# Optimization experiments

Hardware: AMD Instinct MI355X
Metric: run time of the kernel (lower is better)

Reference implementation:

```python
import jax, jax.numpy as jnp
import numpy as np

N, E, D = 50000, 1600000, 32
P = 2.0  # exponent self.p


def setup_inputs() -> dict:
    key = jax.random.key(0)
    k1, k2, k3 = jax.random.split(key, 3)
    X = jax.random.normal(k1, (N, D), dtype=jnp.float32)
    edge_index = jax.random.randint(k2, (2, E), 0, N)
    W = jax.random.normal(k3, (D, D), dtype=jnp.float32) / np.float32(np.sqrt(D))
    b = jnp.zeros((D,), dtype=jnp.float32)
    return {"X": X, "edge_index": edge_index, "W": W, "b": b}


def gcn_conv(X, edge_index, W, b, n):
    # PyG GCNConv: add self-loops, symmetric deg^-1/2 normalization,
    # aggregate messages from source col -> target row.
    src, dst = edge_index[0], edge_index[1]
    loops = jnp.arange(n)
    row = jnp.concatenate([dst, loops])  # targets
    col = jnp.concatenate([src, loops])  # sources
    deg = jax.ops.segment_sum(jnp.ones(row.shape, X.dtype), row, num_segments=n)
    dinv = jax.lax.rsqrt(jnp.maximum(deg, 1.0))  # deg >= 1 (self-loops)
    h = X @ W  # [N, D]
    msg = h[col] * (dinv[col] * dinv[row])[:, None]  # [E+N, D]
    return jax.ops.segment_sum(msg, row, num_segments=n) + b


def reference(X, edge_index, W, b):
    n = X.shape[0]
    h = jax.nn.relu(gcn_conv(X, edge_index, W, b, n))  # activation(conv(X, ei))
    src, dst = edge_index[0], edge_index[1]
    e = jnp.abs(h[src] - h[dst]) ** P  # [E, D] gather + pow
    s = jax.ops.segment_sum(e, src, num_segments=n)  # scatter-sum by source
    cnt = jax.ops.segment_sum(jnp.ones((e.shape[0],), h.dtype), src, num_segments=n)
    mean = s / jnp.maximum(cnt, 1.0)[:, None]  # scatter-mean finalize
    return jnp.tanh(mean)
```

## Files before the change

kernel.cpp:

```cpp
#include <hip/hip_runtime.h>

#define D 32
#define CSH 7
#define KMASK 127
#define PSH 23
#define PMASK ((1u << PSH) - 1u)
#define NBMAX 512

typedef unsigned int uint;

__device__ inline uint bf16rne(float f) {
    uint u = __float_as_uint(f);
    return (u + 0x7FFFu + ((u >> 16) & 1u)) >> 16;
}
__device__ inline float bf_lo(uint w) { return __uint_as_float(w << 16); }
__device__ inline float bf_hi(uint w) { return __uint_as_float(w & 0xFFFF0000u); }
__device__ inline uint bf_pack(float x, float y) { return bf16rne(x) | (bf16rne(y) << 16); }

__global__ void zero_kernel(int* __restrict__ p, int n) {
    int i = threadIdx.x;
    if (i < n) p[i] = 0;
}

__global__ void coarse_scatter(const int* __restrict__ src, const int* __restrict__ dst,
                               int* __restrict__ gCurD, int* __restrict__ gCurS,
                               uint* __restrict__ coarseD, uint* __restrict__ coarseS,
                               int E, int cap) {
    __shared__ int hD[NBMAX], hS[NBMAX], baseD[NBMAX], baseS[NBMAX];
    int t = threadIdx.x;
    if (t < NBMAX) { hD[t] = 0; hS[t] = 0; }
    __syncthreads();
    int s[4], d[4], lpD[4], lpS[4];
    int j0 = blockIdx.x * 4096 + 4 * t;
    int nv = 0;
    if (j0 + 3 < E) {
        int4 s4 = *(const int4*)(src + j0);
        int4 d4 = *(const int4*)(dst + j0);
        s[0] = s4.x; s[1] = s4.y; s[2] = s4.z; s[3] = s4.w;
        d[0] = d4.x; d[1] = d4.y; d[2] = d4.z; d[3] = d4.w;
        nv = 4;
    } else {
        for (int u = 0; u < 4; ++u) {
            int j = j0 + u;
            if (j < E) { s[nv] = src[j]; d[nv] = dst[j]; ++nv; }
        }
    }
    for (int u = 0; u < nv; ++u) {
        lpD[u] = atomicAdd(&hD[d[u] >> CSH], 1);
        lpS[u] = atomicAdd(&hS[s[u] >> CSH], 1);
    }
    __syncthreads();
    if (t < NBMAX) {
        if (hD[t]) baseD[t] = atomicAdd(&gCurD[t], hD[t]);
        if (hS[t]) baseS[t] = atomicAdd(&gCurS[t], hS[t]);
    }
    __syncthreads();
    for (int u = 0; u < nv; ++u) {
        int bD = d[u] >> CSH, relD = baseD[bD] + lpD[u];
        if (relD < cap)
            coarseD[(size_t)bD * cap + relD] = ((uint)(d[u] & KMASK) << PSH) | (uint)s[u];
        int bS = s[u] >> CSH, relS = baseS[bS] + lpS[u];
        if (relS < cap)
            coarseS[(size_t)bS * cap + relS] = ((uint)(s[u] & KMASK) << PSH) | (uint)d[u];
    }
}

__global__ void fineD_build(const uint* __restrict__ coarseD, const int* __restrict__ gCurD,
                            int* __restrict__ rowStartD, int* __restrict__ rowEndD,
                            int* __restrict__ adjD, float* __restrict__ dinv,
                            int N, int cap) {
    __shared__ int cnt[128];
    __shared__ int pre[128];
    int b = blockIdx.x;
    int t = threadIdx.x;
    int nodeLo = b << CSH;
    int nNodes = min(128, N - nodeLo);
    if (t < 128) cnt[t] = 0;
    __syncthreads();
    size_t lo = (size_t)b * cap;
    int n = min(gCurD[b], cap - 512);
    int n4 = n >> 2;
    const uint4* c4 = (const uint4*)(coarseD + lo);
    for (int kk = t; kk < n4; kk += 1024) {
        uint4 e4 = c4[kk];
        atomicAdd(&cnt[e4.x >> PSH], 1);
        atomicAdd(&cnt[e4.y >> PSH], 1);
        atomicAdd(&cnt[e4.z >> PSH], 1);
        atomicAdd(&cnt[e4.w >> PSH], 1);
    }
    for (int kk = 4 * n4 + t; kk < n; kk += 1024)
        atomicAdd(&cnt[coarseD[lo + kk] >> PSH], 1);
    __syncthreads();
    int mydeg = 0, mypad = 0;
    if (t < 128) { mydeg = cnt[t]; mypad = (mydeg + 3) & ~3; pre[t] = mypad; }
    __syncthreads();
    for (int off = 1; off < 128; off <<= 1) {
        int x = 0;
        if (t < 128 && t >= off) x = pre[t - off];
        __syncthreads();
        if (t < 128) pre[t] += x;
        __syncthreads();
    }
    int myexcl = 0;
    if (t < 128) myexcl = pre[t] - mypad;
    if (t < nNodes) {
        rowStartD[nodeLo + t] = (int)lo + myexcl;
        rowEndD[nodeLo + t]   = (int)lo + myexcl + mydeg;
        dinv[nodeLo + t] = rsqrtf((float)(mydeg + 1));
    }
    __syncthreads();
    if (t < 128) cnt[t] = (int)lo + myexcl;
    __syncthreads();
    int hiGuard = (int)lo + cap;
    for (int kk = t; kk < n; kk += 1024) {
        uint e = coarseD[lo + kk];
        int pos = atomicAdd(&cnt[e >> PSH], 1);
        if (pos < hiGuard) adjD[pos] = (int)(e & PMASK);
    }
}

__global__ void matmul_scale_kernel(const float* __restrict__ X, const float* __restrict__ W,
                                    const float* __restrict__ dinv, uint* __restrict__ hs16,
                                    int N) {
    __shared__ float Wl[D * D];
    __shared__ float Xl[8 * D];
    int tid = threadIdx.x;
    for (int k = tid; k < D * D; k += 256) Wl[k] = W[k];
    int row0 = blockIdx.x * 8;
    int g = row0 * D + tid;
    Xl[tid] = (g < N * D) ? X[g] : 0.f;
    __syncthreads();
    int r = tid >> 5;
    int d = tid & 31;
    int row = row0 + r;
    float acc = 0.f;
    #pragma unroll
    for (int k = 0; k < D; ++k) acc += Xl[r * D + k] * Wl[k * D + d];
    if (row < N) acc *= dinv[row];
    float other = __shfl_xor(acc, 1);
    if (row < N && (d & 1) == 0)
        hs16[row * 16 + (d >> 1)] = bf_pack(acc, other);
}

__global__ void conv_gather_kernel(const int* __restrict__ rowStartD, const int* __restrict__ rowEndD,
                                   const int* __restrict__ adjD,
                                   const uint* __restrict__ hs16, const float* __restrict__ dinv,
                                   const float* __restrict__ b, uint* __restrict__ h2_16, int N) {
    int node = blockIdx.x * 8 + (threadIdx.x >> 6);
    if (node >= N) return;
    int lane = threadIdx.x & 63;
    int p = lane & 15;
    int slot = lane >> 4;
    int s = rowStartD[node], e = rowEndD[node];
    float ax0 = 0.f, ay0 = 0.f, ax1 = 0.f, ay1 = 0.f;
    float ax2 = 0.f, ay2 = 0.f, ax3 = 0.f, ay3 = 0.f;
    int k = s;
    for (; k + 15 < e; k += 16) {
        int4 iv = *(const int4*)(adjD + k + slot * 4);
        uint w0 = hs16[iv.x * 16 + p];
        uint w1 = hs16[iv.y * 16 + p];
        uint w2 = hs16[iv.z * 16 + p];
        uint w3 = hs16[iv.w * 16 + p];
        ax0 += bf_lo(w0); ay0 += bf_hi(w0);
        ax1 += bf_lo(w1); ay1 += bf_hi(w1);
        ax2 += bf_lo(w2); ay2 += bf_hi(w2);
        ax3 += bf_lo(w3); ay3 += bf_hi(w3);
    }
    for (; k < e; k += 4) {
        int kk = k + slot;
        if (kk < e) {
            uint w = hs16[adjD[kk] * 16 + p];
            ax0 += bf_lo(w); ay0 += bf_hi(w);
        }
    }
    float accx = (ax0 + ax1) + (ax2 + ax3);
    float accy = (ay0 + ay1) + (ay2 + ay3);
    accx += __shfl_xor(accx, 16); accy += __shfl_xor(accy, 16);
    accx += __shfl_xor(accx, 32); accy += __shfl_xor(accy, 32);
    if (slot == 0) {
        uint wself = hs16[node * 16 + p];
        float di = dinv[node];
        float vx = di * (accx + bf_lo(wself)) + b[2 * p];
        float vy = di * (accy + bf_hi(wself)) + b[2 * p + 1];
        h2_16[node * 16 + p] = bf_pack(fmaxf(vx, 0.f), fmaxf(vy, 0.f));
    }
}

__global__ void __launch_bounds__(1024)
pow_fused(const uint* __restrict__ coarseS, const int* __restrict__ gCurS,
          const uint* __restrict__ h2_16, float* __restrict__ out, int N, int cap) {
    extern __shared__ uint adjL[];
    __shared__ int cnt[128];
    __shared__ int pre[128];
    __shared__ int rs[128];
    __shared__ int degL[128];
    __shared__ uint self[128 * 16];
    int b = blockIdx.x;
    int t = threadIdx.x;
    int nodeLo = b << CSH;
    int nNodes = min(128, N - nodeLo);
    if (t < 128) cnt[t] = 0;
    for (int i = t; i < nNodes * 16; i += 1024)
        self[i] = h2_16[(size_t)(nodeLo + (i >> 4)) * 16 + (i & 15)];
    __syncthreads();
    size_t lo = (size_t)b * cap;
    int n = min(gCurS[b], cap - 512);
    int n4 = n >> 2;
    const uint4* c4 = (const uint4*)(coarseS + lo);
    for (int kk = t; kk < n4; kk += 1024) {
        uint4 e4 = c4[kk];
        atomicAdd(&cnt[e4.x >> PSH], 1);
        atomicAdd(&cnt[e4.y >> PSH], 1);
        atomicAdd(&cnt[e4.z >> PSH], 1);
        atomicAdd(&cnt[e4.w >> PSH], 1);
    }
    for (int kk = 4 * n4 + t; kk < n; kk += 1024)
        atomicAdd(&cnt[coarseS[lo + kk] >> PSH], 1);
    __syncthreads();
    int mydeg = 0, mypad = 0;
    if (t < 128) { mydeg = cnt[t]; mypad = (mydeg + 3) & ~3; pre[t] = mypad; }
    __syncthreads();
    for (int off = 1; off < 128; off <<= 1) {
        int x = 0;
        if (t < 128 && t >= off) x = pre[t - off];
        __syncthreads();
        if (t < 128) pre[t] += x;
        __syncthreads();
    }
    if (t < 128) {
        rs[t] = pre[t] - mypad;
        degL[t] = mydeg;
        cnt[t] = pre[t] - mypad;
    }
    __syncthreads();
    for (int kk = t; kk < n; kk += 1024) {
        uint e = coarseS[lo + kk];
        int pos = atomicAdd(&cnt[e >> PSH], 1);
        if (pos < cap) adjL[pos] = e & PMASK;
    }
    __syncthreads();
    int wave = t >> 6, lane = t & 63;
    int p = lane & 15, slot = lane >> 4;
    for (int nl = wave; nl < nNodes; nl += 16) {
        int s = rs[nl];
        int e = s + degL[nl];
        uint wh = self[nl * 16 + p];
        float hx = bf_lo(wh), hy = bf_hi(wh);
        float ax0 = 0.f, ay0 = 0.f, ax1 = 0.f, ay1 = 0.f;
        float ax2 = 0.f, ay2 = 0.f, ax3 = 0.f, ay3 = 0.f;
        int k = s;
        for (; k + 15 < e; k += 16) {
            uint4 iv = *(const uint4*)(adjL + k + slot * 4);
            uint w0 = h2_16[iv.x * 16 + p];
            uint w1 = h2_16[iv.y * 16 + p];
            uint w2 = h2_16[iv.z * 16 + p];
            uint w3 = h2_16[iv.w * 16 + p];
            float vx0 = hx - bf_lo(w0), vy0 = hy - bf_hi(w0);
            float vx1 = hx - bf_lo(w1), vy1 = hy - bf_hi(w1);
            float vx2 = hx - bf_lo(w2), vy2 = hy - bf_hi(w2);
            float vx3 = hx - bf_lo(w3), vy3 = hy - bf_hi(w3);
            ax0 += vx0 * vx0; ay0 += vy0 * vy0;
            ax1 += vx1 * vx1; ay1 += vy1 * vy1;
            ax2 += vx2 * vx2; ay2 += vy2 * vy2;
            ax3 += vx3 * vx3; ay3 += vy3 * vy3;
        }
        for (; k < e; k += 4) {
            int kk = k + slot;
            if (kk < e) {
                uint w = h2_16[adjL[kk] * 16 + p];
                float vx = hx - bf_lo(w), vy = hy - bf_hi(w);
                ax0 += vx * vx; ay0 += vy * vy;
            }
        }
        float accx = (ax0 + ax1) + (ax2 + ax3);
        float accy = (ay0 + ay1) + (ay2 + ay3);
        accx += __shfl_xor(accx, 16); accy += __shfl_xor(accy, 16);
        accx += __shfl_xor(accx, 32); accy += __shfl_xor(accy, 32);
        if (slot == 0) {
            float c = fmaxf((float)degL[nl], 1.f);
            float2 r;
            r.x = tanhf(accx / c);
            r.y = tanhf(accy / c);
            ((float2*)out)[(size_t)(nodeLo + nl) * 16 + p] = r;
        }
    }
}

__global__ void fb_count(const int* __restrict__ src, const int* __restrict__ dst,
                         int* __restrict__ degI, int* __restrict__ cntI, int E) {
    int j = blockIdx.x * blockDim.x + threadIdx.x;
    if (j < E) {
        atomicAdd(&degI[dst[j]], 1);
        atomicAdd(&cntI[src[j]], 1);
    }
}
__global__ void fb_dinv(const int* __restrict__ degI, float* __restrict__ dinv, int N) {
    int i = blockIdx.x * blockDim.x + threadIdx.x;
    if (i < N) dinv[i] = rsqrtf((float)(degI[i] + 1));
}
__global__ void fb_matmul(const float* __restrict__ X, const float* __restrict__ W,
                          const float* __restrict__ dinv, float* __restrict__ hs, int N) {
    __shared__ float Wl[D * D];
    __shared__ float Xl[8 * D];
    int tid = threadIdx.x;
    for (int k = tid; k < D * D; k += 256) Wl[k] = W[k];
    int row0 = blockIdx.x * 8;
    int g = row0 * D + tid;
    Xl[tid] = (g < N * D) ? X[g] : 0.f;
    __syncthreads();
    int r = tid >> 5;
    int d = tid & 31;
    int row = row0 + r;
    if (row < N) {
        float acc = 0.f;
        #pragma unroll
        for (int k = 0; k < D; ++k) acc += Xl[r * D + k] * Wl[k * D + d];
        hs[row * D + d] = acc * dinv[row];
    }
}
__global__ void fb_scatter_conv(const int* __restrict__ src, const int* __restrict__ dst,
                                const float* __restrict__ hs, float* __restrict__ S, int ED) {
    int idx = blockIdx.x * blockDim.x + threadIdx.x;
    if (idx < ED) {
        int j = idx >> 5, d = idx & 31;
        atomicAdd(&S[dst[j] * D + d], hs[src[j] * D + d]);
    }
}
__global__ void fb_h2(float* __restrict__ S, const float* __restrict__ hs,
                      const float* __restrict__ dinv, const float* __restrict__ b, int ND) {
    int idx = blockIdx.x * blockDim.x + threadIdx.x;
    if (idx < ND) {
        int i = idx >> 5, d = idx & 31;
        float v = dinv[i] * (S[idx] + hs[idx]) + b[d];
        S[idx] = fmaxf(v, 0.f);
    }
}
__global__ void fb_edge_pow(const int* __restrict__ src, const int* __restrict__ dst,
                            const float* __restrict__ h2, float* __restrict__ out, int ED) {
    int idx = blockIdx.x * blockDim.x + threadIdx.x;
    if (idx < ED) {
        int j = idx >> 5, d = idx & 31;
        float v = h2[src[j] * D + d] - h2[dst[j] * D + d];
        atomicAdd(&out[src[j] * D + d], v * v);
    }
}
__global__ void fb_finalize(float* __restrict__ out, const int* __restrict__ cntI, int ND) {
    int idx = blockIdx.x * blockDim.x + threadIdx.x;
    if (idx < ND) {
        int i = idx >> 5;
        float c = fmaxf((float)cntI[i], 1.f);
        out[idx] = tanhf(out[idx] / c);
    }
}

extern "C" void kernel_launch(void* const* d_in, const int* in_sizes, int n_in,
                              void* d_out, int out_size, void* d_ws, size_t ws_size,
                              hipStream_t stream) {
    const float* X  = (const float*)d_in[0];
    const int*   ei = (const int*)d_in[1];
    const float* W  = (const float*)d_in[2];
    const float* b  = (const float*)d_in[3];
    int N = in_sizes[0] / D;
    int E = in_sizes[1] / 2;
    const int* src = ei;
    const int* dst = ei + E;
    float* out = (float*)d_out;

    size_t ND = (size_t)N * D;
    size_t NH = (size_t)N * 16;
    int nb = (N + 127) >> CSH;
    int cap = ((E + nb - 1) / nb + 1024 + 15) & ~15;
    size_t capSz = (size_t)nb * cap;
    size_t ldsBytes = (size_t)cap * 4;

    uint* coarseD = (uint*)d_ws;
    uint* coarseS = coarseD + capSz;
    int* adjD = (int*)(coarseS + capSz);
    uint* hs16   = (uint*)(adjD + capSz);
    uint* h2_16  = hs16 + NH;
    float* dinv = (float*)(h2_16 + NH);
    int* rowStartD = (int*)(dinv + N);
    int* rowEndD   = rowStartD + N;
    int* gCurD  = rowEndD + N;
    int* gCurS  = gCurD + NBMAX;
    size_t need = (3 * capSz + 2 * NH + 3 * (size_t)N + 2 * NBMAX) * 4;

    if (ws_size >= need && nb <= NBMAX && N <= (1 << PSH) && capSz < (1u << 30)
        && ldsBytes <= 96 * 1024) {
        zero_kernel<<<1, 1024, 0, stream>>>(gCurD, 2 * NBMAX);
        int cgrid = (E + 4095) / 4096;
        coarse_scatter<<<cgrid, 1024, 0, stream>>>(src, dst, gCurD, gCurS,
                                                   coarseD, coarseS, E, cap);
        fineD_build<<<nb, 1024, 0, stream>>>(coarseD, gCurD, rowStartD, rowEndD,
                                             adjD, dinv, N, cap);
        matmul_scale_kernel<<<(N + 7) / 8, 256, 0, stream>>>(X, W, dinv, hs16, N);
        conv_gather_kernel<<<(N + 7) / 8, 512, 0, stream>>>(rowStartD, rowEndD, adjD,
                                                            hs16, dinv, b, h2_16, N);
        pow_fused<<<nb, 1024, ldsBytes, stream>>>(coarseS, gCurS, h2_16, out, N, cap);
    } else {
        float* fhs  = (float*)d_ws;
        float* S    = fhs + ND;
        float* fdv  = S + ND;
        int*   fdeg = (int*)(fdv + N);
        int*   fcnt = fdeg + N;
        hipMemsetAsync(S, 0, ND * sizeof(float), stream);
        hipMemsetAsync(fdeg, 0, (size_t)2 * N * sizeof(int), stream);
        hipMemsetAsync(d_out, 0, ND * sizeof(float), stream);
        int EDi = E * D, NDi = (int)ND;
        fb_count<<<(E + 255) / 256, 256, 0, stream>>>(src, dst, fdeg, fcnt, E);
        fb_dinv<<<(N + 255) / 256, 256, 0, stream>>>(fdeg, fdv, N);
        fb_matmul<<<(N + 7) / 8, 256, 0, stream>>>(X, W, fdv, fhs, N);
        fb_scatter_conv<<<(EDi + 255) / 256, 256, 0, stream>>>(src, dst, fhs, S, EDi);
        fb_h2<<<(NDi + 255) / 256, 256, 0, stream>>>(S, fhs, fdv, b, NDi);
        fb_edge_pow<<<(EDi + 255) / 256, 256, 0, stream>>>(src, dst, S, out, EDi);
        fb_finalize<<<(NDi + 255) / 256, 256, 0, stream>>>(out, fcnt, NDi);
    }
}
```

Measured before the change: 109.7 us.

## Fuse CSR fine-bucket build into conv gather using LDS adjacency

```diff
diff --git a/kernel.cpp b/kernel.cpp
--- a/kernel.cpp
+++ b/kernel.cpp
@@ -65,16 +65,10 @@
     }
 }
 
-__global__ void fineD_build(const uint* __restrict__ coarseD, const int* __restrict__ gCurD,
-                            int* __restrict__ rowStartD, int* __restrict__ rowEndD,
-                            int* __restrict__ adjD, float* __restrict__ dinv,
-                            int N, int cap) {
+__global__ void deg_dinv_kernel(const uint* __restrict__ coarseD, const int* __restrict__ gCurD,
+                                float* __restrict__ dinv, int N, int cap) {
     __shared__ int cnt[128];
-    __shared__ int pre[128];
-    int b = blockIdx.x;
-    int t = threadIdx.x;
-    int nodeLo = b << CSH;
-    int nNodes = min(128, N - nodeLo);
+    int b = blockIdx.x, t = threadIdx.x;
     if (t < 128) cnt[t] = 0;
     __syncthreads();
     size_t lo = (size_t)b * cap;
@@ -91,32 +85,8 @@
     for (int kk = 4 * n4 + t; kk < n; kk += 1024)
         atomicAdd(&cnt[coarseD[lo + kk] >> PSH], 1);
     __syncthreads();
-    int mydeg = 0, mypad = 0;
-    if (t < 128) { mydeg = cnt[t]; mypad = (mydeg + 3) & ~3; pre[t] = mypad; }
-    __syncthreads();
-    for (int off = 1; off < 128; off <<= 1) {
-        int x = 0;
-        if (t < 128 && t >= off) x = pre[t - off];
-        __syncthreads();
-        if (t < 128) pre[t] += x;
-        __syncthreads();
-    }
-    int myexcl = 0;
-    if (t < 128) myexcl = pre[t] - mypad;
-    if (t < nNodes) {
-        rowStartD[nodeLo + t] = (int)lo + myexcl;
-        rowEndD[nodeLo + t]   = (int)lo + myexcl + mydeg;
-        dinv[nodeLo + t] = rsqrtf((float)(mydeg + 1));
-    }
-    __syncthreads();
-    if (t < 128) cnt[t] = (int)lo + myexcl;
-    __syncthreads();
-    int hiGuard = (int)lo + cap;
-    for (int kk = t; kk < n; kk += 1024) {
-        uint e = coarseD[lo + kk];
-        int pos = atomicAdd(&cnt[e >> PSH], 1);
-        if (pos < hiGuard) adjD[pos] = (int)(e & PMASK);
-    }
+    int node = (b << CSH) + t;
+    if (t < 128 && node < N) dinv[node] = rsqrtf((float)(cnt[t] + 1));
 }
 
 __global__ void matmul_scale_kernel(const float* __restrict__ X, const float* __restrict__ W,
@@ -142,47 +112,95 @@
         hs16[row * 16 + (d >> 1)] = bf_pack(acc, other);
 }
 
-__global__ void conv_gather_kernel(const int* __restrict__ rowStartD, const int* __restrict__ rowEndD,
-                                   const int* __restrict__ adjD,
-                                   const uint* __restrict__ hs16, const float* __restrict__ dinv,
-                                   const float* __restrict__ b, uint* __restrict__ h2_16, int N) {
-    int node = blockIdx.x * 8 + (threadIdx.x >> 6);
-    if (node >= N) return;
-    int lane = threadIdx.x & 63;
-    int p = lane & 15;
-    int slot = lane >> 4;
-    int s = rowStartD[node], e = rowEndD[node];
-    float ax0 = 0.f, ay0 = 0.f, ax1 = 0.f, ay1 = 0.f;
-    float ax2 = 0.f, ay2 = 0.f, ax3 = 0.f, ay3 = 0.f;
-    int k = s;
-    for (; k + 15 < e; k += 16) {
-        int4 iv = *(const int4*)(adjD + k + slot * 4);
-        uint w0 = hs16[iv.x * 16 + p];
-        uint w1 = hs16[iv.y * 16 + p];
-        uint w2 = hs16[iv.z * 16 + p];
-        uint w3 = hs16[iv.w * 16 + p];
-        ax0 += bf_lo(w0); ay0 += bf_hi(w0);
-        ax1 += bf_lo(w1); ay1 += bf_hi(w1);
-        ax2 += bf_lo(w2); ay2 += bf_hi(w2);
-        ax3 += bf_lo(w3); ay3 += bf_hi(w3);
-    }
-    for (; k < e; k += 4) {
-        int kk = k + slot;
-        if (kk < e) {
-            uint w = hs16[adjD[kk] * 16 + p];
-            ax0 += bf_lo(w); ay0 += bf_hi(w);
-        }
-    }
-    float accx = (ax0 + ax1) + (ax2 + ax3);
-    float accy = (ay0 + ay1) + (ay2 + ay3);
-    accx += __shfl_xor(accx, 16); accy += __shfl_xor(accy, 16);
-    accx += __shfl_xor(accx, 32); accy += __shfl_xor(accy, 32);
-    if (slot == 0) {
-        uint wself = hs16[node * 16 + p];
-        float di = dinv[node];
-        float vx = di * (accx + bf_lo(wself)) + b[2 * p];
-        float vy = di * (accy + bf_hi(wself)) + b[2 * p + 1];
-        h2_16[node * 16 + p] = bf_pack(fmaxf(vx, 0.f), fmaxf(vy, 0.f));
+__global__ void __launch_bounds__(1024)
+conv_fused(const uint* __restrict__ coarseD, const int* __restrict__ gCurD,
+           const uint* __restrict__ hs16, const float* __restrict__ bias,
+           uint* __restrict__ h2_16, int N, int cap) {
+    extern __shared__ uint adjL[];
+    __shared__ int cnt[128];
+    __shared__ int pre[128];
+    __shared__ int rs[128];
+    __shared__ int degL[128];
+    int b = blockIdx.x;
+    int t = threadIdx.x;
+    int nodeLo = b << CSH;
+    int nNodes = min(128, N - nodeLo);
+    if (t < 128) cnt[t] = 0;
+    __syncthreads();
+    size_t lo = (size_t)b * cap;
+    int n = min(gCurD[b], cap - 512);
+    int n4 = n >> 2;
+    const uint4* c4 = (const uint4*)(coarseD + lo);
+    for (int kk = t; kk < n4; kk += 1024) {
+        uint4 e4 = c4[kk];
+        atomicAdd(&cnt[e4.x >> PSH], 1);
+        atomicAdd(&cnt[e4.y >> PSH], 1);
+        atomicAdd(&cnt[e4.z >> PSH], 1);
+        atomicAdd(&cnt[e4.w >> PSH], 1);
+    }
+    for (int kk = 4 * n4 + t; kk < n; kk += 1024)
+        atomicAdd(&cnt[coarseD[lo + kk] >> PSH], 1);
+    __syncthreads();
+    int mydeg = 0, mypad = 0;
+    if (t < 128) { mydeg = cnt[t]; mypad = (mydeg + 3) & ~3; pre[t] = mypad; }
+    __syncthreads();
+    for (int off = 1; off < 128; off <<= 1) {
+        int x = 0;
+        if (t < 128 && t >= off) x = pre[t - off];
+        __syncthreads();
+        if (t < 128) pre[t] += x;
+        __syncthreads();
+    }
+    if (t < 128) {
+        rs[t] = pre[t] - mypad;
+        degL[t] = mydeg;
+        cnt[t] = pre[t] - mypad;
+    }
+    __syncthreads();
+    for (int kk = t; kk < n; kk += 1024) {
+        uint e = coarseD[lo + kk];
+        int pos = atomicAdd(&cnt[e >> PSH], 1);
+        if (pos < cap) adjL[pos] = e & PMASK;
+    }
+    __syncthreads();
+    int wave = t >> 6, lane = t & 63;
+    int p = lane & 15, slot = lane >> 4;
+    for (int nl = wave; nl < nNodes; nl += 16) {
+        int s = rs[nl];
+        int e = s + degL[nl];
+        float ax0 = 0.f, ay0 = 0.f, ax1 = 0.f, ay1 = 0.f;
+        float ax2 = 0.f, ay2 = 0.f, ax3 = 0.f, ay3 = 0.f;
+        int k = s;
+        for (; k + 15 < e; k += 16) {
+            uint4 iv = *(const uint4*)(adjL + k + slot * 4);
+            uint w0 = hs16[iv.x * 16 + p];
+            uint w1 = hs16[iv.y * 16 + p];
+            uint w2 = hs16[iv.z * 16 + p];
+            uint w3 = hs16[iv.w * 16 + p];
+            ax0 += bf_lo(w0); ay0 += bf_hi(w0);
+            ax1 += bf_lo(w1); ay1 += bf_hi(w1);
+            ax2 += bf_lo(w2); ay2 += bf_hi(w2);
+            ax3 += bf_lo(w3); ay3 += bf_hi(w3);
+        }
+        for (; k < e; k += 4) {
+            int kk = k + slot;
+            if (kk < e) {
+                uint w = hs16[adjL[kk] * 16 + p];
+                ax0 += bf_lo(w); ay0 += bf_hi(w);
+            }
+        }
+        float accx = (ax0 + ax1) + (ax2 + ax3);
+        float accy = (ay0 + ay1) + (ay2 + ay3);
+        accx += __shfl_xor(accx, 16); accy += __shfl_xor(accy, 16);
+        accx += __shfl_xor(accx, 32); accy += __shfl_xor(accy, 32);
+        if (slot == 0) {
+            int node = nodeLo + nl;
+            uint wself = hs16[(size_t)node * 16 + p];
+            float di = rsqrtf((float)(degL[nl] + 1));
+            float vx = di * (accx + bf_lo(wself)) + bias[2 * p];
+            float vy = di * (accy + bf_hi(wself)) + bias[2 * p + 1];
+            h2_16[(size_t)node * 16 + p] = bf_pack(fmaxf(vx, 0.f), fmaxf(vy, 0.f));
+        }
     }
 }
 
@@ -375,15 +393,12 @@
 
     uint* coarseD = (uint*)d_ws;
     uint* coarseS = coarseD + capSz;
-    int* adjD = (int*)(coarseS + capSz);
-    uint* hs16   = (uint*)(adjD + capSz);
+    uint* hs16   = coarseS + capSz;
     uint* h2_16  = hs16 + NH;
     float* dinv = (float*)(h2_16 + NH);
-    int* rowStartD = (int*)(dinv + N);
-    int* rowEndD   = rowStartD + N;
-    int* gCurD  = rowEndD + N;
+    int* gCurD  = (int*)(dinv + N);
     int* gCurS  = gCurD + NBMAX;
-    size_t need = (3 * capSz + 2 * NH + 3 * (size_t)N + 2 * NBMAX) * 4;
+    size_t need = (2 * capSz + 2 * NH + (size_t)N + 2 * NBMAX) * 4;
 
     if (ws_size >= need && nb <= NBMAX && N <= (1 << PSH) && capSz < (1u << 30)
         && ldsBytes <= 96 * 1024) {
@@ -391,11 +406,9 @@
         int cgrid = (E + 4095) / 4096;
         coarse_scatter<<<cgrid, 1024, 0, stream>>>(src, dst, gCurD, gCurS,
                                                    coarseD, coarseS, E, cap);
-        fineD_build<<<nb, 1024, 0, stream>>>(coarseD, gCurD, rowStartD, rowEndD,
-                                             adjD, dinv, N, cap);
+        deg_dinv_kernel<<<nb, 1024, 0, stream>>>(coarseD, gCurD, dinv, N, cap);
         matmul_scale_kernel<<<(N + 7) / 8, 256, 0, stream>>>(X, W, dinv, hs16, N);
-        conv_gather_kernel<<<(N + 7) / 8, 512, 0, stream>>>(rowStartD, rowEndD, adjD,
-                                                            hs16, dinv, b, h2_16, N);
+        conv_fused<<<nb, 1024, ldsBytes, stream>>>(coarseD, gCurD, hs16, b, h2_16, N, cap);
         pow_fused<<<nb, 1024, ldsBytes, stream>>>(coarseS, gCurS, h2_16, out, N, cap);
     } else {
         float* fhs  = (float*)d_ws;
```

Measured after the change: 98.18 us. 10.5% less time.
